# Kernel tuning notes

Measured on AMD Instinct MI355X. Metric: run time of the kernel, lower is better.

Reference implementation:

```python
import jax, jax.numpy as jnp
import numpy as np

H = 1024          # hidden_size
V = 50257         # output_size (vocab)
L = 100           # max_length


def setup_inputs() -> dict:
    key = jax.random.key(0)
    ks = jax.random.split(key, 16)
    s = 0.02
    return {
        "input": jax.random.randint(ks[0], (1,), 0, V, dtype=jnp.int64),
        "hidden": jax.random.normal(ks[1], (1, 1, H), dtype=jnp.float32),
        "encoder_outputs": jax.random.normal(ks[2], (L, H), dtype=jnp.float32),
        # parameters
        "emb": jax.random.normal(ks[3], (V, H), dtype=jnp.float32) * s,
        "attn_W": jax.random.normal(ks[4], (L, 2 * H), dtype=jnp.float32) * s,
        "attn_b": jnp.zeros((L,), dtype=jnp.float32),
        "comb_W": jax.random.normal(ks[5], (H, 2 * H), dtype=jnp.float32) * s,
        "comb_b": jnp.zeros((H,), dtype=jnp.float32),
        "W_ih": jax.random.normal(ks[6], (3 * H, H), dtype=jnp.float32) * s,
        "W_hh": jax.random.normal(ks[7], (3 * H, H), dtype=jnp.float32) * s,
        "b_ih": jnp.zeros((3 * H,), dtype=jnp.float32),
        "b_hh": jnp.zeros((3 * H,), dtype=jnp.float32),
        "out_W": jax.random.normal(ks[8], (V, H), dtype=jnp.float32) * s,
        "out_b": jnp.zeros((V,), dtype=jnp.float32),
    }


def reference(input, hidden, encoder_outputs, emb, attn_W, attn_b,
              comb_W, comb_b, W_ih, W_hh, b_ih, b_hh, out_W, out_b):
    # embedding lookup -> [1, H]; dropout is identity at inference
    embedded = emb[input].reshape(1, H)
    h0 = hidden[0]                                     # [1, H]
    # Bahdanau-style attention over fixed max_length positions
    attn_logits = jnp.concatenate([embedded, h0], axis=1) @ attn_W.T + attn_b
    attn_weights = jax.nn.softmax(attn_logits, axis=1)  # [1, L]
    context = attn_weights @ encoder_outputs            # [1, H]
    # combine + relu
    x = jnp.concatenate([embedded, context], axis=1) @ comb_W.T + comb_b
    x = jax.nn.relu(x)                                  # [1, H]
    # single-step GRU (PyTorch gate order: r, z, n)
    gi = x @ W_ih.T + b_ih                              # [1, 3H]
    gh = h0 @ W_hh.T + b_hh                             # [1, 3H]
    i_r, i_z, i_n = jnp.split(gi, 3, axis=1)
    h_r, h_z, h_n = jnp.split(gh, 3, axis=1)
    r = jax.nn.sigmoid(i_r + h_r)
    z = jax.nn.sigmoid(i_z + h_z)
    n = jnp.tanh(i_n + r * h_n)
    h_new = (1.0 - z) * n + z * h0                      # [1, H]
    # output projection + log_softmax
    logits = h_new @ out_W.T + out_b                    # [1, V]
    out = jax.nn.log_softmax(logits, axis=1)
    return out, h_new[None], attn_weights
```

## Files before the change

kernel.cpp:

```cpp
#include <hip/hip_runtime.h>
#include <math.h>

#define H   1024
#define H2  2048
#define L   100
#define V   50257

#define ROWS_PB 16
#define NBLK_OUT ((V + ROWS_PB - 1) / ROWS_PB)

#define WS_ATT   0
#define WS_CTX   128
#define WS_X     1280
#define WS_HNEW  2304
#define WS_PART  3328
#define WS_C     9728

typedef float floatx4 __attribute__((ext_vector_type(4)));

__device__ __forceinline__ float wave_reduce_sum(float v) {
#pragma unroll
    for (int off = 32; off > 0; off >>= 1) v += __shfl_down(v, off);
    return v;
}

__global__ void k_attn_logits(const int* __restrict__ tok,
                              const float* __restrict__ hidden,
                              const float* __restrict__ emb,
                              const float* __restrict__ attn_W,
                              const float* __restrict__ attn_b,
                              float* __restrict__ ws) {
    const int l = blockIdx.x;
    const int t = threadIdx.x;
    const float* __restrict__ row = attn_W + (size_t)l * H2;
    const float* __restrict__ e   = emb + (size_t)tok[0] * H;
    float acc = 0.f;
#pragma unroll
    for (int base = 0; base < H2; base += 1024) {
        int i = base + t * 4;
        float4 w = *(const float4*)(row + i);
        const float* __restrict__ src = (i < H) ? (e + i) : (hidden + (i - H));
        float4 v = *(const float4*)src;
        acc += w.x * v.x + w.y * v.y + w.z * v.z + w.w * v.w;
    }
    acc = wave_reduce_sum(acc);
    __shared__ float sh[4];
    if ((t & 63) == 0) sh[t >> 6] = acc;
    __syncthreads();
    if (t == 0) ws[WS_ATT + l] = sh[0] + sh[1] + sh[2] + sh[3] + attn_b[l];
}

__global__ void k_ctx(const float* __restrict__ enc,
                      float* __restrict__ ws,
                      float* __restrict__ out) {
    const int t = threadIdx.x;
    __shared__ float sl[128];
    __shared__ float shw[L];
    float v = (t < L) ? ws[WS_ATT + t] : -INFINITY;
    sl[t] = v;
    __syncthreads();
    for (int s = 64; s > 0; s >>= 1) {
        if (t < s) sl[t] = fmaxf(sl[t], sl[t + s]);
        __syncthreads();
    }
    float m = sl[0];
    __syncthreads();
    float e = (t < L) ? expf(v - m) : 0.f;
    sl[t] = e;
    __syncthreads();
    for (int s = 64; s > 0; s >>= 1) {
        if (t < s) sl[t] += sl[t + s];
        __syncthreads();
    }
    float denom = sl[0];
    if (t < L) {
        float w = e / denom;
        shw[t] = w;
        if (blockIdx.x == 0) out[V + H + t] = w;
    }
    __syncthreads();
    const int h = blockIdx.x * 128 + t;
    float acc = 0.f;
#pragma unroll 4
    for (int l = 0; l < L; ++l) acc += shw[l] * enc[(size_t)l * H + h];
    ws[WS_CTX + h] = acc;
}

__global__ void k_combine(const int* __restrict__ tok,
                          const float* __restrict__ emb,
                          const float* __restrict__ comb_W,
                          const float* __restrict__ comb_b,
                          float* __restrict__ ws) {
    const int t = threadIdx.x;
    const int wave = t >> 6, lane = t & 63;
    const int j = blockIdx.x * 4 + wave;
    const float* __restrict__ e   = emb + (size_t)tok[0] * H;
    const float* __restrict__ ctx = ws + WS_CTX;
    const float* __restrict__ row = comb_W + (size_t)j * H2;
    float acc = 0.f;
#pragma unroll
    for (int it = 0; it < 8; ++it) {
        int i = it * 256 + lane * 4;
        float4 w = *(const float4*)(row + i);
        const float* __restrict__ src = (i < H) ? (e + i) : (ctx + (i - H));
        float4 v = *(const float4*)src;
        acc += w.x * v.x + w.y * v.y + w.z * v.z + w.w * v.w;
    }
    acc = wave_reduce_sum(acc);
    if (lane == 0) ws[WS_X + j] = fmaxf(acc + comb_b[j], 0.f);
}

__global__ void k_gru(const float* __restrict__ hidden,
                      const float* __restrict__ W_ih,
                      const float* __restrict__ W_hh,
                      const float* __restrict__ b_ih,
                      const float* __restrict__ b_hh,
                      float* __restrict__ ws,
                      float* __restrict__ out) {
    const int j = blockIdx.x;
    const int t = threadIdx.x;
    const int w = t >> 6, lane = t & 63;
    const float* __restrict__ vec = (w < 3) ? (ws + WS_X) : hidden;
    const float* __restrict__ row = (w < 3)
        ? (W_ih + ((size_t)w * H + j) * H)
        : (W_hh + ((size_t)(w - 3) * H + j) * H);
    float acc = 0.f;
#pragma unroll
    for (int it = 0; it < 4; ++it) {
        int i = it * 256 + lane * 4;
        float4 a = *(const float4*)(row + i);
        float4 v = *(const float4*)(vec + i);
        acc += a.x * v.x + a.y * v.y + a.z * v.z + a.w * v.w;
    }
    acc = wave_reduce_sum(acc);
    __shared__ float sh[6];
    if (lane == 0) sh[w] = acc;
    __syncthreads();
    if (t == 0) {
        float ir  = sh[0] + b_ih[j];
        float iz  = sh[1] + b_ih[H + j];
        float inn = sh[2] + b_ih[2 * H + j];
        float hr  = sh[3] + b_hh[j];
        float hz  = sh[4] + b_hh[H + j];
        float hn  = sh[5] + b_hh[2 * H + j];
        float r = 1.f / (1.f + expf(-(ir + hr)));
        float z = 1.f / (1.f + expf(-(iz + hz)));
        float n = tanhf(inn + r * hn);
        float hnew = (1.f - z) * n + z * hidden[j];
        out[V + j]      = hnew;
        ws[WS_HNEW + j] = hnew;
    }
}

__global__ void k_out_gemv(const float* __restrict__ out_W,
                           const float* __restrict__ out_b,
                           const float* __restrict__ ws,
                           float* __restrict__ out,
                           float* __restrict__ part) {
    __shared__ float shv[H];
    __shared__ float slog[ROWS_PB];
    const int t = threadIdx.x;
    *(float4*)(shv + t * 4) = *(const float4*)(ws + WS_HNEW + t * 4);
    __syncthreads();
    const int wave = t >> 6, lane = t & 63;
    const int r0 = blockIdx.x * ROWS_PB + wave * 4;
    const float* __restrict__ base = out_W + (size_t)r0 * H;
    float acc0 = 0.f, acc1 = 0.f, acc2 = 0.f, acc3 = 0.f;
    if (r0 + 3 < V) {
#pragma unroll
        for (int it = 0; it < 4; ++it) {
            const int i = it * 256 + lane * 4;
            float4 b = *(const float4*)(shv + i);
            floatx4 a0 = __builtin_nontemporal_load((const floatx4*)(base + i));
            floatx4 a1 = __builtin_nontemporal_load((const floatx4*)(base + H + i));
            floatx4 a2 = __builtin_nontemporal_load((const floatx4*)(base + 2 * H + i));
            floatx4 a3 = __builtin_nontemporal_load((const floatx4*)(base + 3 * H + i));
            acc0 += a0.x * b.x + a0.y * b.y + a0.z * b.z + a0.w * b.w;
            acc1 += a1.x * b.x + a1.y * b.y + a1.z * b.z + a1.w * b.w;
            acc2 += a2.x * b.x + a2.y * b.y + a2.z * b.z + a2.w * b.w;
            acc3 += a3.x * b.x + a3.y * b.y + a3.z * b.z + a3.w * b.w;
        }
    } else {
        for (int it = 0; it < 4; ++it) {
            const int i = it * 256 + lane * 4;
            float4 b = *(const float4*)(shv + i);
            if (r0 + 0 < V) { float4 a = *(const float4*)(base + i);
                acc0 += a.x * b.x + a.y * b.y + a.z * b.z + a.w * b.w; }
            if (r0 + 1 < V) { float4 a = *(const float4*)(base + H + i);
                acc1 += a.x * b.x + a.y * b.y + a.z * b.z + a.w * b.w; }
            if (r0 + 2 < V) { float4 a = *(const float4*)(base + 2 * H + i);
                acc2 += a.x * b.x + a.y * b.y + a.z * b.z + a.w * b.w; }
            if (r0 + 3 < V) { float4 a = *(const float4*)(base + 3 * H + i);
                acc3 += a.x * b.x + a.y * b.y + a.z * b.z + a.w * b.w; }
        }
    }
    acc0 = wave_reduce_sum(acc0);
    acc1 = wave_reduce_sum(acc1);
    acc2 = wave_reduce_sum(acc2);
    acc3 = wave_reduce_sum(acc3);
    if (lane == 0) {
        float lg[4] = {acc0, acc1, acc2, acc3};
#pragma unroll
        for (int r = 0; r < 4; ++r) {
            int row = r0 + r;
            float l = (row < V) ? lg[r] + out_b[row] : -INFINITY;
            if (row < V) out[row] = l;
            slog[wave * 4 + r] = l;
        }
    }
    __syncthreads();
    if (t == 0) {
        float m = slog[0];
#pragma unroll
        for (int i = 1; i < ROWS_PB; ++i) m = fmaxf(m, slog[i]);
        float s = 0.f;
#pragma unroll
        for (int i = 0; i < ROWS_PB; ++i) s += expf(slog[i] - m);
        part[2 * blockIdx.x]     = m;
        part[2 * blockIdx.x + 1] = s;
    }
}

__global__ void k_lse(const float* __restrict__ part, float* __restrict__ ws) {
    const int t = threadIdx.x;
    float m = -INFINITY, s = 0.f;
    for (int i = t; i < NBLK_OUT; i += 256) {
        float pm = part[2 * i], ps = part[2 * i + 1];
        if (pm > m) { s = s * expf(m - pm) + ps; m = pm; }
        else        { s += ps * expf(pm - m); }
    }
#pragma unroll
    for (int off = 32; off > 0; off >>= 1) {
        float m2 = __shfl_down(m, off);
        float s2 = __shfl_down(s, off);
        float M = fmaxf(m, m2);
        s = s * expf(m - M) + s2 * expf(m2 - M);
        m = M;
    }
    __shared__ float shm[4], shs[4];
    const int wave = t >> 6, lane = t & 63;
    if (lane == 0) { shm[wave] = m; shs[wave] = s; }
    __syncthreads();
    if (t == 0) {
        float M = shm[0], S = shs[0];
        for (int i = 1; i < 4; ++i) {
            float M2 = fmaxf(M, shm[i]);
            S = S * expf(M - M2) + shs[i] * expf(shm[i] - M2);
            M = M2;
        }
        ws[WS_C] = M + logf(S);
    }
}

__global__ void k_sub(float* __restrict__ out, const float* __restrict__ ws) {
    const int v = blockIdx.x * 256 + threadIdx.x;
    if (v < V) out[v] -= ws[WS_C];
}

extern "C" void kernel_launch(void* const* d_in, const int* in_sizes, int n_in,
                              void* d_out, int out_size, void* d_ws, size_t ws_size,
                              hipStream_t stream) {
    const int*   tok    = (const int*)d_in[0];
    const float* hidden = (const float*)d_in[1];
    const float* enc    = (const float*)d_in[2];
    const float* emb    = (const float*)d_in[3];
    const float* attn_W = (const float*)d_in[4];
    const float* attn_b = (const float*)d_in[5];
    const float* comb_W = (const float*)d_in[6];
    const float* comb_b = (const float*)d_in[7];
    const float* W_ih   = (const float*)d_in[8];
    const float* W_hh   = (const float*)d_in[9];
    const float* b_ih   = (const float*)d_in[10];
    const float* b_hh   = (const float*)d_in[11];
    const float* out_W  = (const float*)d_in[12];
    const float* out_b  = (const float*)d_in[13];
    float* out = (float*)d_out;
    float* ws  = (float*)d_ws;

    k_attn_logits<<<L, 256, 0, stream>>>(tok, hidden, emb, attn_W, attn_b, ws);
    k_ctx<<<8, 128, 0, stream>>>(enc, ws, out);
    k_combine<<<256, 256, 0, stream>>>(tok, emb, comb_W, comb_b, ws);
    k_gru<<<H, 384, 0, stream>>>(hidden, W_ih, W_hh, b_ih, b_hh, ws, out);
    k_out_gemv<<<NBLK_OUT, 256, 0, stream>>>(out_W, out_b, ws, out, ws + WS_PART);
    k_lse<<<1, 256, 0, stream>>>(ws + WS_PART, ws);
    k_sub<<<(V + 255) / 256, 256, 0, stream>>>(out, ws);
}
```

Before: 420.2 us.

## Fuse all decoder stages into one persistent cooperative kernel with grid syncs

```diff
diff --git a/kernel.cpp b/kernel.cpp
--- a/kernel.cpp
+++ b/kernel.cpp
@@ -1,20 +1,22 @@
 #include <hip/hip_runtime.h>
+#include <hip/hip_cooperative_groups.h>
 #include <math.h>
+
+namespace cg = cooperative_groups;
 
 #define H   1024
 #define H2  2048
 #define L   100
 #define V   50257
-
-#define ROWS_PB 16
-#define NBLK_OUT ((V + ROWS_PB - 1) / ROWS_PB)
+#define NB  512
+#define BS  256
 
 #define WS_ATT   0
 #define WS_CTX   128
 #define WS_X     1280
-#define WS_HNEW  2304
-#define WS_PART  3328
-#define WS_C     9728
+#define WS_GI    2304
+#define WS_HNEW  8448
+#define WS_PART  9472
 
 typedef float floatx4 __attribute__((ext_vector_type(4)));
 
@@ -24,125 +26,138 @@
     return v;
 }
 
-__global__ void k_attn_logits(const int* __restrict__ tok,
-                              const float* __restrict__ hidden,
-                              const float* __restrict__ emb,
-                              const float* __restrict__ attn_W,
-                              const float* __restrict__ attn_b,
-                              float* __restrict__ ws) {
-    const int l = blockIdx.x;
+__device__ __forceinline__ float dot4(const float4 a, const float4 b) {
+    return a.x * b.x + a.y * b.y + a.z * b.z + a.w * b.w;
+}
+
+__global__ __launch_bounds__(BS, 2)
+void k_fused(const int* __restrict__ tok,
+             const float* __restrict__ hidden,
+             const float* __restrict__ enc,
+             const float* __restrict__ emb,
+             const float* __restrict__ attn_W,
+             const float* __restrict__ attn_b,
+             const float* __restrict__ comb_W,
+             const float* __restrict__ comb_b,
+             const float* __restrict__ W_ih,
+             const float* __restrict__ W_hh,
+             const float* __restrict__ b_ih,
+             const float* __restrict__ b_hh,
+             const float* __restrict__ out_W,
+             const float* __restrict__ out_b,
+             float* __restrict__ out,
+             float* __restrict__ ws) {
+    cg::grid_group grid = cg::this_grid();
+    const int b = blockIdx.x;
     const int t = threadIdx.x;
-    const float* __restrict__ row = attn_W + (size_t)l * H2;
-    const float* __restrict__ e   = emb + (size_t)tok[0] * H;
-    float acc = 0.f;
-#pragma unroll
-    for (int base = 0; base < H2; base += 1024) {
-        int i = base + t * 4;
-        float4 w = *(const float4*)(row + i);
-        const float* __restrict__ src = (i < H) ? (e + i) : (hidden + (i - H));
-        float4 v = *(const float4*)src;
-        acc += w.x * v.x + w.y * v.y + w.z * v.z + w.w * v.w;
-    }
-    acc = wave_reduce_sum(acc);
-    __shared__ float sh[4];
-    if ((t & 63) == 0) sh[t >> 6] = acc;
-    __syncthreads();
-    if (t == 0) ws[WS_ATT + l] = sh[0] + sh[1] + sh[2] + sh[3] + attn_b[l];
-}
-
-__global__ void k_ctx(const float* __restrict__ enc,
-                      float* __restrict__ ws,
-                      float* __restrict__ out) {
-    const int t = threadIdx.x;
+    const int wave = t >> 6, lane = t & 63;
+    const float* __restrict__ e = emb + (size_t)tok[0] * H;
+
+    __shared__ float shv[H];
     __shared__ float sl[128];
     __shared__ float shw[L];
-    float v = (t < L) ? ws[WS_ATT + t] : -INFINITY;
-    sl[t] = v;
-    __syncthreads();
-    for (int s = 64; s > 0; s >>= 1) {
-        if (t < s) sl[t] = fmaxf(sl[t], sl[t + s]);
-        __syncthreads();
-    }
-    float m = sl[0];
-    __syncthreads();
-    float e = (t < L) ? expf(v - m) : 0.f;
-    sl[t] = e;
-    __syncthreads();
-    for (int s = 64; s > 0; s >>= 1) {
-        if (t < s) sl[t] += sl[t + s];
-        __syncthreads();
-    }
-    float denom = sl[0];
-    if (t < L) {
-        float w = e / denom;
-        shw[t] = w;
-        if (blockIdx.x == 0) out[V + H + t] = w;
-    }
-    __syncthreads();
-    const int h = blockIdx.x * 128 + t;
-    float acc = 0.f;
+    __shared__ float red[8];
+
+    if (b < L) {
+        const float* __restrict__ row = attn_W + (size_t)b * H2;
+        const int i = t * 4;
+        float4 w0 = *(const float4*)(row + i);
+        float4 v0 = *(const float4*)(e + i);
+        float4 w1 = *(const float4*)(row + H + i);
+        float4 v1 = *(const float4*)(hidden + i);
+        float acc = dot4(w0, v0) + dot4(w1, v1);
+        acc = wave_reduce_sum(acc);
+        if (lane == 0) red[wave] = acc;
+        __syncthreads();
+        if (t == 0) ws[WS_ATT + b] = red[0] + red[1] + red[2] + red[3] + attn_b[b];
+    }
+    grid.sync();
+
+    if (b < 8) {
+        float v = 0.f, ex = 0.f;
+        if (t < 128) { v = (t < L) ? ws[WS_ATT + t] : -INFINITY; sl[t] = v; }
+        __syncthreads();
+        for (int s = 64; s > 0; s >>= 1) {
+            if (t < s) sl[t] = fmaxf(sl[t], sl[t + s]);
+            __syncthreads();
+        }
+        float m = sl[0];
+        __syncthreads();
+        if (t < 128) { ex = (t < L) ? expf(v - m) : 0.f; sl[t] = ex; }
+        __syncthreads();
+        for (int s = 64; s > 0; s >>= 1) {
+            if (t < s) sl[t] += sl[t + s];
+            __syncthreads();
+        }
+        float denom = sl[0];
+        if (t < L) {
+            float w = ex / denom;
+            shw[t] = w;
+            if (b == 0) out[V + H + t] = w;
+        }
+        __syncthreads();
+        if (t < 128) {
+            const int h = b * 128 + t;
+            float acc = 0.f;
 #pragma unroll 4
-    for (int l = 0; l < L; ++l) acc += shw[l] * enc[(size_t)l * H + h];
-    ws[WS_CTX + h] = acc;
-}
-
-__global__ void k_combine(const int* __restrict__ tok,
-                          const float* __restrict__ emb,
-                          const float* __restrict__ comb_W,
-                          const float* __restrict__ comb_b,
-                          float* __restrict__ ws) {
-    const int t = threadIdx.x;
-    const int wave = t >> 6, lane = t & 63;
-    const int j = blockIdx.x * 4 + wave;
-    const float* __restrict__ e   = emb + (size_t)tok[0] * H;
-    const float* __restrict__ ctx = ws + WS_CTX;
-    const float* __restrict__ row = comb_W + (size_t)j * H2;
-    float acc = 0.f;
-#pragma unroll
-    for (int it = 0; it < 8; ++it) {
-        int i = it * 256 + lane * 4;
-        float4 w = *(const float4*)(row + i);
-        const float* __restrict__ src = (i < H) ? (e + i) : (ctx + (i - H));
-        float4 v = *(const float4*)src;
-        acc += w.x * v.x + w.y * v.y + w.z * v.z + w.w * v.w;
-    }
-    acc = wave_reduce_sum(acc);
-    if (lane == 0) ws[WS_X + j] = fmaxf(acc + comb_b[j], 0.f);
-}
-
-__global__ void k_gru(const float* __restrict__ hidden,
-                      const float* __restrict__ W_ih,
-                      const float* __restrict__ W_hh,
-                      const float* __restrict__ b_ih,
-                      const float* __restrict__ b_hh,
-                      float* __restrict__ ws,
-                      float* __restrict__ out) {
-    const int j = blockIdx.x;
-    const int t = threadIdx.x;
-    const int w = t >> 6, lane = t & 63;
-    const float* __restrict__ vec = (w < 3) ? (ws + WS_X) : hidden;
-    const float* __restrict__ row = (w < 3)
-        ? (W_ih + ((size_t)w * H + j) * H)
-        : (W_hh + ((size_t)(w - 3) * H + j) * H);
-    float acc = 0.f;
-#pragma unroll
-    for (int it = 0; it < 4; ++it) {
-        int i = it * 256 + lane * 4;
-        float4 a = *(const float4*)(row + i);
-        float4 v = *(const float4*)(vec + i);
-        acc += a.x * v.x + a.y * v.y + a.z * v.z + a.w * v.w;
-    }
-    acc = wave_reduce_sum(acc);
-    __shared__ float sh[6];
-    if (lane == 0) sh[w] = acc;
-    __syncthreads();
-    if (t == 0) {
-        float ir  = sh[0] + b_ih[j];
-        float iz  = sh[1] + b_ih[H + j];
-        float inn = sh[2] + b_ih[2 * H + j];
-        float hr  = sh[3] + b_hh[j];
-        float hz  = sh[4] + b_hh[H + j];
-        float hn  = sh[5] + b_hh[2 * H + j];
+            for (int l = 0; l < L; ++l) acc += shw[l] * enc[(size_t)l * H + h];
+            ws[WS_CTX + h] = acc;
+        }
+    }
+    grid.sync();
+
+    if (b < 256) {
+        const int j = b * 4 + wave;
+        const float* __restrict__ ctx = ws + WS_CTX;
+        const float* __restrict__ row = comb_W + (size_t)j * H2;
+        float acc = 0.f;
+#pragma unroll
+        for (int it = 0; it < 8; ++it) {
+            const int i = it * 256 + lane * 4;
+            float4 w = *(const float4*)(row + i);
+            const float* __restrict__ src = (i < H) ? (e + i) : (ctx + (i - H));
+            float4 v = *(const float4*)src;
+            acc += dot4(w, v);
+        }
+        acc = wave_reduce_sum(acc);
+        if (lane == 0) ws[WS_X + j] = fmaxf(acc + comb_b[j], 0.f);
+    }
+    grid.sync();
+
+    {
+        const int g = b * 4 + wave;
+#pragma unroll
+        for (int it = 0; it < 3; ++it) {
+            const int task = it * 2048 + g;
+            const int gate = task >> 10;
+            const int j = task & 1023;
+            const float* __restrict__ vec = (gate < 3) ? (ws + WS_X) : hidden;
+            const float* __restrict__ row = (gate < 3)
+                ? (W_ih + ((size_t)gate * H + j) * H)
+                : (W_hh + ((size_t)(gate - 3) * H + j) * H);
+            float acc = 0.f;
+#pragma unroll
+            for (int k = 0; k < 4; ++k) {
+                const int i = k * 256 + lane * 4;
+                float4 a = *(const float4*)(row + i);
+                float4 v = *(const float4*)(vec + i);
+                acc += dot4(a, v);
+            }
+            acc = wave_reduce_sum(acc);
+            if (lane == 0) ws[WS_GI + task] = acc;
+        }
+    }
+    grid.sync();
+
+    if (b < 4) {
+        const int j = b * 256 + t;
+        const float* __restrict__ gi = ws + WS_GI;
+        float ir  = gi[j]            + b_ih[j];
+        float iz  = gi[H + j]        + b_ih[H + j];
+        float inn = gi[2 * H + j]    + b_ih[2 * H + j];
+        float hr  = gi[3 * H + j]    + b_hh[j];
+        float hz  = gi[4 * H + j]    + b_hh[H + j];
+        float hn  = gi[5 * H + j]    + b_hh[2 * H + j];
         float r = 1.f / (1.f + expf(-(ir + hr)));
         float z = 1.f / (1.f + expf(-(iz + hz)));
         float n = tanhf(inn + r * hn);
@@ -150,111 +165,110 @@
         out[V + j]      = hnew;
         ws[WS_HNEW + j] = hnew;
     }
-}
-
-__global__ void k_out_gemv(const float* __restrict__ out_W,
-                           const float* __restrict__ out_b,
-                           const float* __restrict__ ws,
-                           float* __restrict__ out,
-                           float* __restrict__ part) {
-    __shared__ float shv[H];
-    __shared__ float slog[ROWS_PB];
-    const int t = threadIdx.x;
-    *(float4*)(shv + t * 4) = *(const float4*)(ws + WS_HNEW + t * 4);
-    __syncthreads();
-    const int wave = t >> 6, lane = t & 63;
-    const int r0 = blockIdx.x * ROWS_PB + wave * 4;
-    const float* __restrict__ base = out_W + (size_t)r0 * H;
-    float acc0 = 0.f, acc1 = 0.f, acc2 = 0.f, acc3 = 0.f;
-    if (r0 + 3 < V) {
-#pragma unroll
-        for (int it = 0; it < 4; ++it) {
-            const int i = it * 256 + lane * 4;
-            float4 b = *(const float4*)(shv + i);
-            floatx4 a0 = __builtin_nontemporal_load((const floatx4*)(base + i));
-            floatx4 a1 = __builtin_nontemporal_load((const floatx4*)(base + H + i));
-            floatx4 a2 = __builtin_nontemporal_load((const floatx4*)(base + 2 * H + i));
-            floatx4 a3 = __builtin_nontemporal_load((const floatx4*)(base + 3 * H + i));
-            acc0 += a0.x * b.x + a0.y * b.y + a0.z * b.z + a0.w * b.w;
-            acc1 += a1.x * b.x + a1.y * b.y + a1.z * b.z + a1.w * b.w;
-            acc2 += a2.x * b.x + a2.y * b.y + a2.z * b.z + a2.w * b.w;
-            acc3 += a3.x * b.x + a3.y * b.y + a3.z * b.z + a3.w * b.w;
-        }
-    } else {
-        for (int it = 0; it < 4; ++it) {
-            const int i = it * 256 + lane * 4;
-            float4 b = *(const float4*)(shv + i);
-            if (r0 + 0 < V) { float4 a = *(const float4*)(base + i);
-                acc0 += a.x * b.x + a.y * b.y + a.z * b.z + a.w * b.w; }
-            if (r0 + 1 < V) { float4 a = *(const float4*)(base + H + i);
-                acc1 += a.x * b.x + a.y * b.y + a.z * b.z + a.w * b.w; }
-            if (r0 + 2 < V) { float4 a = *(const float4*)(base + 2 * H + i);
-                acc2 += a.x * b.x + a.y * b.y + a.z * b.z + a.w * b.w; }
-            if (r0 + 3 < V) { float4 a = *(const float4*)(base + 3 * H + i);
-                acc3 += a.x * b.x + a.y * b.y + a.z * b.z + a.w * b.w; }
-        }
-    }
-    acc0 = wave_reduce_sum(acc0);
-    acc1 = wave_reduce_sum(acc1);
-    acc2 = wave_reduce_sum(acc2);
-    acc3 = wave_reduce_sum(acc3);
-    if (lane == 0) {
-        float lg[4] = {acc0, acc1, acc2, acc3};
-#pragma unroll
-        for (int r = 0; r < 4; ++r) {
-            int row = r0 + r;
-            float l = (row < V) ? lg[r] + out_b[row] : -INFINITY;
-            if (row < V) out[row] = l;
-            slog[wave * 4 + r] = l;
-        }
-    }
-    __syncthreads();
-    if (t == 0) {
-        float m = slog[0];
-#pragma unroll
-        for (int i = 1; i < ROWS_PB; ++i) m = fmaxf(m, slog[i]);
-        float s = 0.f;
-#pragma unroll
-        for (int i = 0; i < ROWS_PB; ++i) s += expf(slog[i] - m);
-        part[2 * blockIdx.x]     = m;
-        part[2 * blockIdx.x + 1] = s;
-    }
-}
-
-__global__ void k_lse(const float* __restrict__ part, float* __restrict__ ws) {
-    const int t = threadIdx.x;
-    float m = -INFINITY, s = 0.f;
-    for (int i = t; i < NBLK_OUT; i += 256) {
-        float pm = part[2 * i], ps = part[2 * i + 1];
-        if (pm > m) { s = s * expf(m - pm) + ps; m = pm; }
-        else        { s += ps * expf(pm - m); }
-    }
-#pragma unroll
-    for (int off = 32; off > 0; off >>= 1) {
-        float m2 = __shfl_down(m, off);
-        float s2 = __shfl_down(s, off);
-        float M = fmaxf(m, m2);
-        s = s * expf(m - M) + s2 * expf(m2 - M);
-        m = M;
-    }
-    __shared__ float shm[4], shs[4];
-    const int wave = t >> 6, lane = t & 63;
-    if (lane == 0) { shm[wave] = m; shs[wave] = s; }
-    __syncthreads();
-    if (t == 0) {
-        float M = shm[0], S = shs[0];
-        for (int i = 1; i < 4; ++i) {
-            float M2 = fmaxf(M, shm[i]);
-            S = S * expf(M - M2) + shs[i] * expf(shm[i] - M2);
-            M = M2;
-        }
-        ws[WS_C] = M + logf(S);
-    }
-}
-
-__global__ void k_sub(float* __restrict__ out, const float* __restrict__ ws) {
-    const int v = blockIdx.x * 256 + threadIdx.x;
-    if (v < V) out[v] -= ws[WS_C];
+    grid.sync();
+
+    {
+        *(float4*)(shv + t * 4) = *(const float4*)(ws + WS_HNEW + t * 4);
+        __syncthreads();
+        const int g = b * 4 + wave;
+        float m = -INFINITY, s = 0.f;
+#pragma unroll 1
+        for (int pass = 0; pass < 7; ++pass) {
+            const int r0 = (pass * 2048 + g) * 4;
+            if (r0 >= V) break;
+            const float* __restrict__ base = out_W + (size_t)r0 * H;
+            float acc0 = 0.f, acc1 = 0.f, acc2 = 0.f, acc3 = 0.f;
+            if (r0 + 3 < V) {
+#pragma unroll
+                for (int it = 0; it < 4; ++it) {
+                    const int i = it * 256 + lane * 4;
+                    float4 bv = *(const float4*)(shv + i);
+                    floatx4 a0 = __builtin_nontemporal_load((const floatx4*)(base + i));
+                    floatx4 a1 = __builtin_nontemporal_load((const floatx4*)(base + H + i));
+                    floatx4 a2 = __builtin_nontemporal_load((const floatx4*)(base + 2 * H + i));
+                    floatx4 a3 = __builtin_nontemporal_load((const floatx4*)(base + 3 * H + i));
+                    acc0 += a0.x * bv.x + a0.y * bv.y + a0.z * bv.z + a0.w * bv.w;
+                    acc1 += a1.x * bv.x + a1.y * bv.y + a1.z * bv.z + a1.w * bv.w;
+                    acc2 += a2.x * bv.x + a2.y * bv.y + a2.z * bv.z + a2.w * bv.w;
+                    acc3 += a3.x * bv.x + a3.y * bv.y + a3.z * bv.z + a3.w * bv.w;
+                }
+            } else {
+                for (int it = 0; it < 4; ++it) {
+                    const int i = it * 256 + lane * 4;
+                    float4 bv = *(const float4*)(shv + i);
+                    if (r0 + 0 < V) { float4 a = *(const float4*)(base + i);           acc0 += dot4(a, bv); }
+                    if (r0 + 1 < V) { float4 a = *(const float4*)(base + H + i);       acc1 += dot4(a, bv); }
+                    if (r0 + 2 < V) { float4 a = *(const float4*)(base + 2 * H + i);   acc2 += dot4(a, bv); }
+                    if (r0 + 3 < V) { float4 a = *(const float4*)(base + 3 * H + i);   acc3 += dot4(a, bv); }
+                }
+            }
+            acc0 = wave_reduce_sum(acc0);
+            acc1 = wave_reduce_sum(acc1);
+            acc2 = wave_reduce_sum(acc2);
+            acc3 = wave_reduce_sum(acc3);
+            if (lane == 0) {
+                float lg[4] = {acc0, acc1, acc2, acc3};
+#pragma unroll
+                for (int r = 0; r < 4; ++r) {
+                    const int row = r0 + r;
+                    if (row < V) {
+                        float l = lg[r] + out_b[row];
+                        out[row] = l;
+                        if (l > m) { s = s * expf(m - l) + 1.f; m = l; }
+                        else       { s += expf(l - m); }
+                    }
+                }
+            }
+        }
+        __syncthreads();
+        if (lane == 0) { red[wave] = m; red[4 + wave] = s; }
+        __syncthreads();
+        if (t == 0) {
+            float M = red[0], S = red[4];
+#pragma unroll
+            for (int i = 1; i < 4; ++i) {
+                float M2 = fmaxf(M, red[i]);
+                S = S * expf(M - M2) + red[4 + i] * expf(red[i] - M2);
+                M = M2;
+            }
+            ws[WS_PART + 2 * b]     = M;
+            ws[WS_PART + 2 * b + 1] = S;
+        }
+    }
+    grid.sync();
+
+    {
+        const float* __restrict__ part = ws + WS_PART;
+        float m1 = part[2 * t],         s1 = part[2 * t + 1];
+        float m2 = part[2 * (t + 256)], s2 = part[2 * (t + 256) + 1];
+        float m = fmaxf(m1, m2);
+        float s = s1 * expf(m1 - m) + s2 * expf(m2 - m);
+#pragma unroll
+        for (int off = 32; off > 0; off >>= 1) {
+            float mo = __shfl_down(m, off);
+            float so = __shfl_down(s, off);
+            float M = fmaxf(m, mo);
+            s = s * expf(m - M) + so * expf(mo - M);
+            m = M;
+        }
+        __syncthreads();
+        if (lane == 0) { red[wave] = m; red[4 + wave] = s; }
+        __syncthreads();
+        if (t == 0) {
+            float M = red[0], S = red[4];
+#pragma unroll
+            for (int i = 1; i < 4; ++i) {
+                float M2 = fmaxf(M, red[i]);
+                S = S * expf(M - M2) + red[4 + i] * expf(red[i] - M2);
+                M = M2;
+            }
+            sl[0] = M + logf(S);
+        }
+        __syncthreads();
+        const float c = sl[0];
+        const int idx = b * BS + t;
+        if (idx < V) out[idx] -= c;
+    }
 }
 
 extern "C" void kernel_launch(void* const* d_in, const int* in_sizes, int n_in,
@@ -277,11 +291,12 @@
     float* out = (float*)d_out;
     float* ws  = (float*)d_ws;
 
-    k_attn_logits<<<L, 256, 0, stream>>>(tok, hidden, emb, attn_W, attn_b, ws);
-    k_ctx<<<8, 128, 0, stream>>>(enc, ws, out);
-    k_combine<<<256, 256, 0, stream>>>(tok, emb, comb_W, comb_b, ws);
-    k_gru<<<H, 384, 0, stream>>>(hidden, W_ih, W_hh, b_ih, b_hh, ws, out);
-    k_out_gemv<<<NBLK_OUT, 256, 0, stream>>>(out_W, out_b, ws, out, ws + WS_PART);
-    k_lse<<<1, 256, 0, stream>>>(ws + WS_PART, ws);
-    k_sub<<<(V + 255) / 256, 256, 0, stream>>>(out, ws);
+    void* args[] = {
+        (void*)&tok, (void*)&hidden, (void*)&enc, (void*)&emb,
+        (void*)&attn_W, (void*)&attn_b, (void*)&comb_W, (void*)&comb_b,
+        (void*)&W_ih, (void*)&W_hh, (void*)&b_ih, (void*)&b_hh,
+        (void*)&out_W, (void*)&out_b, (void*)&out, (void*)&ws
+    };
+    hipLaunchCooperativeKernel((const void*)k_fused, dim3(NB), dim3(BS),
+                               args, 0, stream);
 }
```

New measurement: 765.0 us. +82.0%, slower.
